# Kernel tuning notes

Measured on AMD Instinct MI355X. Metric: run time of the kernel, lower is better.

## Reference

```python
import jax, jax.numpy as jnp
import numpy as np
from jax import lax

# Problem sizes (see shape_source)
B, N, S, K = 16, 4096, 1024, 32   # clouds, points/cloud, fps samples/cloud, max neighbors
C_IN, H1, H2, C_OUT = 64, 64, 64, 128
R = 0.2                            # radius ball query radius


def setup_inputs() -> dict:
    key = jax.random.key(0)
    ks = jax.random.split(key, 6)
    x = jax.random.normal(ks[0], (B * N, C_IN), jnp.float32)
    pos = jax.random.uniform(ks[1], (B * N, 3), jnp.float32)  # unit cube
    batch = jnp.repeat(jnp.arange(B, dtype=jnp.int32), N)     # equal-size clouds
    def lin(k, fan_in, fan_out):
        return jax.random.normal(k, (fan_in, fan_out), jnp.float32) / np.float32(np.sqrt(fan_in))
    W1 = lin(ks[2], C_IN + 3, H1); b1 = jnp.zeros((H1,), jnp.float32)
    W2 = lin(ks[3], H1, H2);      b2 = jnp.zeros((H2,), jnp.float32)
    W3 = lin(ks[4], H2, C_OUT);   b3 = jnp.zeros((C_OUT,), jnp.float32)
    return dict(x=x, pos=pos, batch=batch, W1=W1, b1=b1, W2=W2, b2=b2, W3=W3, b3=b3)


def _fps_single(pos):
    """Farthest point sampling on one cloud. pos: [N,3] -> [S] int32 indices.
    Deterministic start at index 0 (random_start=False equivalent)."""
    def step(carry, _):
        mind, last = carry
        d = jnp.sum((pos - pos[last]) ** 2, axis=-1)   # [N]
        mind = jnp.minimum(mind, d)
        nxt = jnp.argmax(mind).astype(jnp.int32)
        return (mind, nxt), last
    init = (jnp.full((pos.shape[0],), jnp.inf, pos.dtype), jnp.int32(0))
    _, idx = lax.scan(step, init, None, length=S)
    return idx  # [S]


def _radius_single(pos, qpos):
    """Ball query: for each query return up to K in-radius neighbors (first K by
    point index, matching torch_cluster's 'first found' semantics).
    pos: [N,3], qpos: [S,3] -> (nbr [S,K] int32, mask [S,K] bool)."""
    d2 = jnp.sum((qpos[:, None, :] - pos[None, :, :]) ** 2, axis=-1)   # [S,N]
    valid = d2 <= R * R
    key = jnp.where(valid, jnp.arange(N, dtype=jnp.int32), jnp.int32(N))  # invalid -> sentinel N
    neg_key, nbr = lax.top_k(-key, K)        # K smallest keys == first K valid indices
    mask = (-neg_key) < N
    nbr = jnp.where(mask, nbr, 0).astype(jnp.int32)  # safe gather index
    return nbr, mask


def reference(x, pos, batch, W1, b1, W2, b2, W3, b3):
    xb = x.reshape(B, N, C_IN)
    posb = pos.reshape(B, N, 3)

    # 1) FPS sampling per cloud
    idx = jax.vmap(_fps_single)(posb)                                   # [B,S]
    qpos = jnp.take_along_axis(posb, idx[:, :, None], axis=1)           # [B,S,3]

    # 2) radius ball query (max 32 neighbors)
    nbr, mask = jax.vmap(_radius_single)(posb, qpos)                    # [B,S,K]

    # 3) PointNetConv: gather, relative pos, MLP, masked max-scatter
    flat = nbr.reshape(B, S * K)
    xj = jnp.take_along_axis(xb, flat[:, :, None], axis=1).reshape(B, S, K, C_IN)
    pj = jnp.take_along_axis(posb, flat[:, :, None], axis=1).reshape(B, S, K, 3)
    rel = pj - qpos[:, :, None, :]                                      # pos_j - pos_i
    h = jnp.concatenate([xj, rel], axis=-1)                             # [B,S,K,C_IN+3]
    h = jax.nn.relu(h @ W1 + b1)
    h = jax.nn.relu(h @ W2 + b2)
    h = h @ W3 + b3                                                     # [B,S,K,C_OUT]
    h = jnp.where(mask[..., None], h, -jnp.inf)
    agg = jnp.max(h, axis=2)                                            # max aggregation
    agg = jnp.where(jnp.any(mask, axis=2)[..., None], agg, 0.0)         # empty -> 0
    out = jax.nn.relu(agg)                                              # [B,S,C_OUT]

    new_batch = jnp.repeat(jnp.arange(B, dtype=batch.dtype), S)
    return out.reshape(B * S, C_OUT), qpos.reshape(B * S, 3), new_batch
```

## Files before the change

kernel.cpp:

```cpp
#include <hip/hip_runtime.h>
#include <cstdint>
#include <cstddef>

#define B_    16
#define N_    4096
#define S_    1024
#define K_    32
#define COUT_ 128
#define NQ_   (B_*S_)

#define NBLK_FPS  16
#define NBLK_XW   1024
#define NBLK_CONV 8192
#define GRID_     (NBLK_FPS + NBLK_XW + NBLK_CONV)

union __align__(16) SMem {
  struct {
    float px[N_], py[N_], pz[N_];
    int   hist[S_];
    unsigned long long wkey[2][4];
    float wx[2][4], wy[2][4], wz[2][4];
  } fps;
  struct {
    float xs[64*65];
    float ws[64*64];
  } xw;
  struct {
    float h1s[64*68];
    float h2s[64*68];
    float red[8*128];
    int   nbrs[64];
    float qps[8];
    int   cnts[2];
  } conv;
};

__device__ __forceinline__ uint64_t wave_max_u64_l63(uint64_t key) {
  uint32_t lo = (uint32_t)key, hi = (uint32_t)(key >> 32);
#define DPP_STEP(ctrl) { \
    uint32_t lo2 = (uint32_t)__builtin_amdgcn_update_dpp((int)lo, (int)lo, (ctrl), 0xf, 0xf, false); \
    uint32_t hi2 = (uint32_t)__builtin_amdgcn_update_dpp((int)hi, (int)hi, (ctrl), 0xf, 0xf, false); \
    const bool gt = (hi2 > hi) || (hi2 == hi && lo2 > lo); \
    hi = gt ? hi2 : hi; lo = gt ? lo2 : lo; \
  }
  DPP_STEP(0x111)
  DPP_STEP(0x112)
  DPP_STEP(0x114)
  DPP_STEP(0x118)
  DPP_STEP(0x142)
  DPP_STEP(0x143)
#undef DPP_STEP
  return ((uint64_t)hi << 32) | lo;
}

__device__ __forceinline__ void fps_role(
    SMem& sm, int b, const float* __restrict__ pos,
    float* __restrict__ qpos, float* __restrict__ batchf, int* progress)
{
  const int t = threadIdx.x;
  const int lane = t & 63, wid = t >> 6;
  const float* pb = pos + (size_t)b * N_ * 3;

  for (int i = t; i < N_; i += 256) {
    sm.fps.px[i] = pb[i*3+0]; sm.fps.py[i] = pb[i*3+1]; sm.fps.pz[i] = pb[i*3+2];
  }
  for (int s = t; s < S_; s += 256) batchf[(size_t)b*S_ + s] = (float)b;
  __syncthreads();

  float rx[16], ry[16], rz[16], mind[16];
  #pragma unroll
  for (int k = 0; k < 16; ++k) {
    const int p = k*256 + t;
    rx[k] = sm.fps.px[p]; ry[k] = sm.fps.py[p]; rz[k] = sm.fps.pz[p];
    mind[k] = INFINITY;
  }
  __builtin_amdgcn_s_setprio(2);

  int last = 0;
  float lx = sm.fps.px[0], ly = sm.fps.py[0], lz = sm.fps.pz[0];

  for (int s = 0; s < S_; ++s) {
    if (t == 0) sm.fps.hist[s] = last;
    if (s == S_-1) break;

    float bm = -1.0f; int kb = 0;
    #pragma unroll
    for (int k = 0; k < 16; ++k) {
      #pragma clang fp contract(off)
      const float dx = rx[k]-lx;
      const float dy = ry[k]-ly;
      const float dz = rz[k]-lz;
      const float d  = dx*dx + dy*dy + dz*dz;
      const float m  = fminf(mind[k], d);
      mind[k] = m;
      if (m > bm) { bm = m; kb = k; }
    }
    uint64_t key = ((uint64_t)__float_as_uint(bm) << 32)
                 | (uint32_t)((N_-1) - (kb*256 + t));
    key = wave_max_u64_l63(key);
    const int par = s & 1;
    if (lane == 63) {
      const int p = (N_-1) - (int)(uint32_t)key;
      sm.fps.wkey[par][wid] = key;
      sm.fps.wx[par][wid] = sm.fps.px[p];
      sm.fps.wy[par][wid] = sm.fps.py[p];
      sm.fps.wz[par][wid] = sm.fps.pz[p];
    }
    __syncthreads();
    {
      uint64_t k0 = sm.fps.wkey[par][0], k1 = sm.fps.wkey[par][1];
      uint64_t k2 = sm.fps.wkey[par][2], k3 = sm.fps.wkey[par][3];
      float x0=sm.fps.wx[par][0], x1=sm.fps.wx[par][1], x2=sm.fps.wx[par][2], x3=sm.fps.wx[par][3];
      float y0=sm.fps.wy[par][0], y1=sm.fps.wy[par][1], y2=sm.fps.wy[par][2], y3=sm.fps.wy[par][3];
      float z0=sm.fps.wz[par][0], z1=sm.fps.wz[par][1], z2=sm.fps.wz[par][2], z3=sm.fps.wz[par][3];
      if (k1 > k0) { k0=k1; x0=x1; y0=y1; z0=z1; }
      if (k3 > k2) { k2=k3; x2=x3; y2=y3; z2=z3; }
      if (k2 > k0) { k0=k2; x0=x2; y0=y2; z0=z2; }
      last = (N_-1) - (int)(uint32_t)k0;
      lx = x0; ly = y0; lz = z0;
    }
    if ((s & 31) == 31) {
      if (t < 32) {
        const int row = s - 31 + t;
        const int p = sm.fps.hist[row];
        const size_t o = ((size_t)b*S_ + row)*3;
        qpos[o+0] = sm.fps.px[p];
        qpos[o+1] = sm.fps.py[p];
        qpos[o+2] = sm.fps.pz[p];
      }
      if (t == 0)
        __hip_atomic_store(&progress[b], s+1, __ATOMIC_RELEASE, __HIP_MEMORY_SCOPE_AGENT);
    }
  }
  if (t < 32) {
    const int row = (S_-32) + t;
    const int p = sm.fps.hist[row];
    const size_t o = ((size_t)b*S_ + row)*3;
    qpos[o+0] = sm.fps.px[p];
    qpos[o+1] = sm.fps.py[p];
    qpos[o+2] = sm.fps.pz[p];
  }
  if (t == 0)
    __hip_atomic_store(&progress[b], S_, __ATOMIC_RELEASE, __HIP_MEMORY_SCOPE_AGENT);
}

__device__ __forceinline__ void xw_role(
    SMem& sm, int tile, const float* __restrict__ x,
    const float* __restrict__ W1, float* __restrict__ xw, int* xwdone)
{
  const int t = threadIdx.x;
  const size_t rowbase = (size_t)tile * 64;
  for (int k = t; k < 4096; k += 256) {
    sm.xw.xs[(k >> 6)*65 + (k & 63)] = x[rowbase*64 + k];
    sm.xw.ws[k] = W1[k];
  }
  __syncthreads();
  const int rg = t >> 4, cg = t & 15;
  const int r0 = rg*4, c0 = cg*4;
  float acc[4][4] = {};
  for (int i = 0; i < 64; ++i) {
    const float4 w = *(const float4*)&sm.xw.ws[i*64 + c0];
    #pragma unroll
    for (int j = 0; j < 4; ++j) {
      const float a = sm.xw.xs[(r0+j)*65 + i];
      acc[j][0] = fmaf(a, w.x, acc[j][0]);
      acc[j][1] = fmaf(a, w.y, acc[j][1]);
      acc[j][2] = fmaf(a, w.z, acc[j][2]);
      acc[j][3] = fmaf(a, w.w, acc[j][3]);
    }
  }
  #pragma unroll
  for (int j = 0; j < 4; ++j) {
    float4 v; v.x=acc[j][0]; v.y=acc[j][1]; v.z=acc[j][2]; v.w=acc[j][3];
    *(float4*)&xw[(rowbase + r0 + j)*64 + c0] = v;
  }
  __syncthreads();
  if (t == 0)
    __hip_atomic_fetch_add(&xwdone[tile >> 6], 1, __ATOMIC_RELEASE, __HIP_MEMORY_SCOPE_AGENT);
}

__device__ __forceinline__ void conv_role(
    SMem& sm, int j, const float* __restrict__ pos, const float* __restrict__ qpos,
    const float* __restrict__ xw,
    const float* __restrict__ W1, const float* __restrict__ b1,
    const float* __restrict__ W2, const float* __restrict__ b2,
    const float* __restrict__ W3, const float* __restrict__ b3,
    float* __restrict__ out, int* progress, int* xwdone)
{
  const int t = threadIdx.x;
  const int bb   = j & 15;
  const int pair = j >> 4;
  const int q0   = bb*S_ + pair*2;

  if (t == 0) {
    while (__hip_atomic_load(&xwdone[bb], __ATOMIC_ACQUIRE, __HIP_MEMORY_SCOPE_AGENT) < 64)
      __builtin_amdgcn_s_sleep(127);
    const int need = pair*2 + 2;
    while (__hip_atomic_load(&progress[bb], __ATOMIC_ACQUIRE, __HIP_MEMORY_SCOPE_AGENT) < need)
      __builtin_amdgcn_s_sleep(127);
  }
  __syncthreads();

  const int wid = t >> 6, lane = t & 63;
  if (wid < 2) {
    const int q = q0 + wid;
    const float* pb = pos + (size_t)bb * N_ * 3;
    const float qx = qpos[(size_t)q*3+0];
    const float qy = qpos[(size_t)q*3+1];
    const float qz = qpos[(size_t)q*3+2];
    int cnt = 0;
    for (int base = 0; base < N_; base += 64) {
      #pragma clang fp contract(off)
      const int i = base + lane;
      const float dx = qx - pb[i*3+0];
      const float dy = qy - pb[i*3+1];
      const float dz = qz - pb[i*3+2];
      const float d  = dx*dx + dy*dy + dz*dz;
      const bool valid = (d <= 0.04f);
      const unsigned long long bal = __ballot(valid);
      const int below = __popcll(bal & ((1ull << lane) - 1ull));
      const int p = cnt + below;
      if (valid && p < K_) sm.conv.nbrs[wid*K_ + p] = i;
      cnt += __popcll(bal);
      if (cnt >= K_) break;
    }
    const int c = (cnt < K_) ? cnt : K_;
    if (lane >= c && lane < K_) sm.conv.nbrs[wid*K_ + lane] = 0;
    if (lane == 0) sm.conv.cnts[wid] = c;
  }
  if (t < 6) sm.conv.qps[(t/3)*4 + (t%3)] = qpos[(size_t)q0*3 + t];
  __syncthreads();

  {
    const int c = t & 63;
    const int rsub = t >> 6;
    const float w1x = W1[64*64 + c];
    const float w1y = W1[65*64 + c];
    const float w1z = W1[66*64 + c];
    const float b1v = b1[c];
    #pragma unroll
    for (int it = 0; it < 16; ++it) {
      const int row = it*4 + rsub;
      const int lq  = row >> 5;
      const int jn  = sm.conv.nbrs[row];
      const size_t gp = (size_t)bb*N_ + jn;
      const float xv = xw[gp*64 + c];
      const float rx = pos[gp*3+0] - sm.conv.qps[lq*4+0];
      const float ry = pos[gp*3+1] - sm.conv.qps[lq*4+1];
      const float rz = pos[gp*3+2] - sm.conv.qps[lq*4+2];
      float h = fmaf(rx, w1x, xv);
      h = fmaf(ry, w1y, h);
      h = fmaf(rz, w1z, h);
      h += b1v;
      sm.conv.h1s[row*68 + c] = fmaxf(h, 0.0f);
    }
  }
  __syncthreads();

  {
    const int rg = t >> 4, cg = t & 15;
    const int r0 = rg*4, c0 = cg*4;
    float acc[4][4] = {};
    for (int i = 0; i < 64; i += 4) {
      float a[4][4];
      #pragma unroll
      for (int jj = 0; jj < 4; ++jj)
        *(float4*)&a[jj][0] = *(const float4*)&sm.conv.h1s[(r0+jj)*68 + i];
      #pragma unroll
      for (int di = 0; di < 4; ++di) {
        const float4 w = *(const float4*)&W2[(i+di)*64 + c0];
        #pragma unroll
        for (int jj = 0; jj < 4; ++jj) {
          const float av = a[jj][di];
          acc[jj][0] = fmaf(av, w.x, acc[jj][0]);
          acc[jj][1] = fmaf(av, w.y, acc[jj][1]);
          acc[jj][2] = fmaf(av, w.z, acc[jj][2]);
          acc[jj][3] = fmaf(av, w.w, acc[jj][3]);
        }
      }
    }
    const float4 bbv = *(const float4*)&b2[c0];
    #pragma unroll
    for (int jj = 0; jj < 4; ++jj) {
      float4 v;
      v.x = fmaxf(acc[jj][0] + bbv.x, 0.0f);
      v.y = fmaxf(acc[jj][1] + bbv.y, 0.0f);
      v.z = fmaxf(acc[jj][2] + bbv.z, 0.0f);
      v.w = fmaxf(acc[jj][3] + bbv.w, 0.0f);
      *(float4*)&sm.conv.h2s[(r0+jj)*68 + c0] = v;
    }
  }
  __syncthreads();

  {
    const int rg = t >> 5, cg = t & 31;
    const int r0 = rg*8, c0 = cg*4;
    const int lq = rg >> 2;
    const int cq = sm.conv.cnts[lq];
    float acc[8][4] = {};
    for (int i = 0; i < 64; i += 4) {
      float a[8][4];
      #pragma unroll
      for (int jj = 0; jj < 8; ++jj)
        *(float4*)&a[jj][0] = *(const float4*)&sm.conv.h2s[(r0+jj)*68 + i];
      #pragma unroll
      for (int di = 0; di < 4; ++di) {
        const float4 w = *(const float4*)&W3[(size_t)(i+di)*128 + c0];
        #pragma unroll
        for (int jj = 0; jj < 8; ++jj) {
          const float av = a[jj][di];
          acc[jj][0] = fmaf(av, w.x, acc[jj][0]);
          acc[jj][1] = fmaf(av, w.y, acc[jj][1]);
          acc[jj][2] = fmaf(av, w.z, acc[jj][2]);
          acc[jj][3] = fmaf(av, w.w, acc[jj][3]);
        }
      }
    }
    float pm0=-INFINITY, pm1=-INFINITY, pm2=-INFINITY, pm3=-INFINITY;
    #pragma unroll
    for (int jj = 0; jj < 8; ++jj) {
      const int n = (r0 + jj) & 31;
      if (n < cq) {
        pm0 = fmaxf(pm0, acc[jj][0]);
        pm1 = fmaxf(pm1, acc[jj][1]);
        pm2 = fmaxf(pm2, acc[jj][2]);
        pm3 = fmaxf(pm3, acc[jj][3]);
      }
    }
    float4 v; v.x=pm0; v.y=pm1; v.z=pm2; v.w=pm3;
    *(float4*)&sm.conv.red[rg*128 + c0] = v;
  }
  __syncthreads();
  {
    const int q = t >> 7, c = t & 127;
    const int cq = sm.conv.cnts[q];
    float v = -INFINITY;
    #pragma unroll
    for (int jj = 0; jj < 4; ++jj) v = fmaxf(v, sm.conv.red[(q*4+jj)*128 + c]);
    v = (cq > 0) ? (v + b3[c]) : 0.0f;
    v = fmaxf(v, 0.0f);
    out[(size_t)(q0 + q)*COUT_ + c] = v;
  }
}

__global__ __launch_bounds__(256) void mega_kernel(
    const float* __restrict__ x, const float* __restrict__ pos,
    const float* __restrict__ W1, const float* __restrict__ b1,
    const float* __restrict__ W2, const float* __restrict__ b2,
    const float* __restrict__ W3, const float* __restrict__ b3,
    float* __restrict__ out, float* __restrict__ qpos, float* __restrict__ batchf,
    float* __restrict__ xw, int* flags)
{
  __shared__ SMem sm;
  __shared__ int tk_s;
  int* ticket   = flags + 0;
  int* progress = flags + 16;
  int* xwdone   = flags + 48;
  if (threadIdx.x == 0) tk_s = atomicAdd(ticket, 1);
  __syncthreads();
  const int tk = tk_s;

  if (tk < NBLK_FPS) {
    fps_role(sm, tk, pos, qpos, batchf, progress);
  } else if (tk < NBLK_FPS + NBLK_XW) {
    xw_role(sm, tk - NBLK_FPS, x, W1, xw, xwdone);
  } else {
    conv_role(sm, tk - NBLK_FPS - NBLK_XW, pos, qpos, xw,
              W1, b1, W2, b2, W3, b3, out, progress, xwdone);
  }
}

extern "C" void kernel_launch(void* const* d_in, const int* in_sizes, int n_in,
                              void* d_out, int out_size, void* d_ws, size_t ws_size,
                              hipStream_t stream) {
  const float* x   = (const float*)d_in[0];
  const float* pos = (const float*)d_in[1];
  const float* W1  = (const float*)d_in[3];
  const float* b1  = (const float*)d_in[4];
  const float* W2  = (const float*)d_in[5];
  const float* b2  = (const float*)d_in[6];
  const float* W3  = (const float*)d_in[7];
  const float* b3  = (const float*)d_in[8];

  float* out    = (float*)d_out;
  float* qpos   = out + (size_t)NQ_*COUT_;
  float* batchf = qpos + (size_t)NQ_*3;

  char* ws = (char*)d_ws;
  float* xw  = (float*)ws;
  int* flags = (int*)(ws + (size_t)B_*N_*64*sizeof(float));

  hipMemsetAsync(flags, 0, 256, stream);
  hipLaunchKernelGGL(mega_kernel, dim3(GRID_), dim3(256), 0, stream,
                     x, pos, W1, b1, W2, b2, W3, b3, out, qpos, batchf, xw, flags);
}
```

Before: 1.020 ms.

## Convert mega-kernel to persistent workers with atomic work queues and dedicated FPS CUs

The launch drops from one block per task to 256 resident blocks. Sixteen of them run farthest point sampling; the rest pull XW tiles and then conv items from global atomic counters, waiting on the existing progress flags. The shared-memory union is padded to 88 KB, which limits each CU to one block, so the latency-bound FPS blocks no longer share a CU with conv work; the setprio hint is removed as a result. The cost is less latency hiding for the worker phases and the overhead of a serialized atomic counter for every work item.

```diff
diff --git a/kernel.cpp b/kernel.cpp
--- a/kernel.cpp
+++ b/kernel.cpp
@@ -9,10 +9,16 @@
 #define COUT_ 128
 #define NQ_   (B_*S_)
 
+#define NBLK_     256
 #define NBLK_FPS  16
-#define NBLK_XW   1024
-#define NBLK_CONV 8192
-#define GRID_     (NBLK_FPS + NBLK_XW + NBLK_CONV)
+#define NXW_TILES 1024
+#define NCONV_    8192
+
+#define F_TICKET 0
+#define F_PROG   16
+#define F_XWDONE 32
+#define F_XWCTR  64
+#define F_CVCTR  80
 
 union __align__(16) SMem {
   struct {
@@ -33,6 +39,7 @@
     float qps[8];
     int   cnts[2];
   } conv;
+  char pad[90112];
 };
 
 __device__ __forceinline__ uint64_t wave_max_u64_l63(uint64_t key) {
@@ -55,7 +62,7 @@
 
 __device__ __forceinline__ void fps_role(
     SMem& sm, int b, const float* __restrict__ pos,
-    float* __restrict__ qpos, float* __restrict__ batchf, int* progress)
+    float* __restrict__ qpos, float* __restrict__ batchf, volatile int* flags)
 {
   const int t = threadIdx.x;
   const int lane = t & 63, wid = t >> 6;
@@ -74,50 +81,49 @@
     rx[k] = sm.fps.px[p]; ry[k] = sm.fps.py[p]; rz[k] = sm.fps.pz[p];
     mind[k] = INFINITY;
   }
-  __builtin_amdgcn_s_setprio(2);
 
   int last = 0;
   float lx = sm.fps.px[0], ly = sm.fps.py[0], lz = sm.fps.pz[0];
 
   for (int s = 0; s < S_; ++s) {
     if (t == 0) sm.fps.hist[s] = last;
-    if (s == S_-1) break;
-
-    float bm = -1.0f; int kb = 0;
-    #pragma unroll
-    for (int k = 0; k < 16; ++k) {
-      #pragma clang fp contract(off)
-      const float dx = rx[k]-lx;
-      const float dy = ry[k]-ly;
-      const float dz = rz[k]-lz;
-      const float d  = dx*dx + dy*dy + dz*dz;
-      const float m  = fminf(mind[k], d);
-      mind[k] = m;
-      if (m > bm) { bm = m; kb = k; }
-    }
-    uint64_t key = ((uint64_t)__float_as_uint(bm) << 32)
-                 | (uint32_t)((N_-1) - (kb*256 + t));
-    key = wave_max_u64_l63(key);
-    const int par = s & 1;
-    if (lane == 63) {
-      const int p = (N_-1) - (int)(uint32_t)key;
-      sm.fps.wkey[par][wid] = key;
-      sm.fps.wx[par][wid] = sm.fps.px[p];
-      sm.fps.wy[par][wid] = sm.fps.py[p];
-      sm.fps.wz[par][wid] = sm.fps.pz[p];
-    }
-    __syncthreads();
-    {
-      uint64_t k0 = sm.fps.wkey[par][0], k1 = sm.fps.wkey[par][1];
-      uint64_t k2 = sm.fps.wkey[par][2], k3 = sm.fps.wkey[par][3];
-      float x0=sm.fps.wx[par][0], x1=sm.fps.wx[par][1], x2=sm.fps.wx[par][2], x3=sm.fps.wx[par][3];
-      float y0=sm.fps.wy[par][0], y1=sm.fps.wy[par][1], y2=sm.fps.wy[par][2], y3=sm.fps.wy[par][3];
-      float z0=sm.fps.wz[par][0], z1=sm.fps.wz[par][1], z2=sm.fps.wz[par][2], z3=sm.fps.wz[par][3];
-      if (k1 > k0) { k0=k1; x0=x1; y0=y1; z0=z1; }
-      if (k3 > k2) { k2=k3; x2=x3; y2=y3; z2=z3; }
-      if (k2 > k0) { k0=k2; x0=x2; y0=y2; z0=z2; }
-      last = (N_-1) - (int)(uint32_t)k0;
-      lx = x0; ly = y0; lz = z0;
+    if (s < S_-1) {
+      float bm = -1.0f; int kb = 0;
+      #pragma unroll
+      for (int k = 0; k < 16; ++k) {
+        #pragma clang fp contract(off)
+        const float dx = rx[k]-lx;
+        const float dy = ry[k]-ly;
+        const float dz = rz[k]-lz;
+        const float d  = dx*dx + dy*dy + dz*dz;
+        const float m  = fminf(mind[k], d);
+        mind[k] = m;
+        if (m > bm) { bm = m; kb = k; }
+      }
+      uint64_t key = ((uint64_t)__float_as_uint(bm) << 32)
+                   | (uint32_t)((N_-1) - (kb*256 + t));
+      key = wave_max_u64_l63(key);
+      const int par = s & 1;
+      if (lane == 63) {
+        const int p = (N_-1) - (int)(uint32_t)key;
+        sm.fps.wkey[par][wid] = key;
+        sm.fps.wx[par][wid] = sm.fps.px[p];
+        sm.fps.wy[par][wid] = sm.fps.py[p];
+        sm.fps.wz[par][wid] = sm.fps.pz[p];
+      }
+      __syncthreads();
+      {
+        uint64_t k0 = sm.fps.wkey[par][0], k1 = sm.fps.wkey[par][1];
+        uint64_t k2 = sm.fps.wkey[par][2], k3 = sm.fps.wkey[par][3];
+        float x0=sm.fps.wx[par][0], x1=sm.fps.wx[par][1], x2=sm.fps.wx[par][2], x3=sm.fps.wx[par][3];
+        float y0=sm.fps.wy[par][0], y1=sm.fps.wy[par][1], y2=sm.fps.wy[par][2], y3=sm.fps.wy[par][3];
+        float z0=sm.fps.wz[par][0], z1=sm.fps.wz[par][1], z2=sm.fps.wz[par][2], z3=sm.fps.wz[par][3];
+        if (k1 > k0) { k0=k1; x0=x1; y0=y1; z0=z1; }
+        if (k3 > k2) { k2=k3; x2=x3; y2=y3; z2=z3; }
+        if (k2 > k0) { k0=k2; x0=x2; y0=y2; z0=z2; }
+        last = (N_-1) - (int)(uint32_t)k0;
+        lx = x0; ly = y0; lz = z0;
+      }
     }
     if ((s & 31) == 31) {
       if (t < 32) {
@@ -129,24 +135,14 @@
         qpos[o+2] = sm.fps.pz[p];
       }
       if (t == 0)
-        __hip_atomic_store(&progress[b], s+1, __ATOMIC_RELEASE, __HIP_MEMORY_SCOPE_AGENT);
-    }
-  }
-  if (t < 32) {
-    const int row = (S_-32) + t;
-    const int p = sm.fps.hist[row];
-    const size_t o = ((size_t)b*S_ + row)*3;
-    qpos[o+0] = sm.fps.px[p];
-    qpos[o+1] = sm.fps.py[p];
-    qpos[o+2] = sm.fps.pz[p];
-  }
-  if (t == 0)
-    __hip_atomic_store(&progress[b], S_, __ATOMIC_RELEASE, __HIP_MEMORY_SCOPE_AGENT);
-}
-
-__device__ __forceinline__ void xw_role(
+        __hip_atomic_store((int*)&flags[F_PROG + b], s+1, __ATOMIC_RELEASE, __HIP_MEMORY_SCOPE_AGENT);
+    }
+  }
+}
+
+__device__ __forceinline__ void xw_tile_body(
     SMem& sm, int tile, const float* __restrict__ x,
-    const float* __restrict__ W1, float* __restrict__ xw, int* xwdone)
+    const float* __restrict__ W1, float* __restrict__ xw)
 {
   const int t = threadIdx.x;
   const size_t rowbase = (size_t)tile * 64;
@@ -174,34 +170,19 @@
     float4 v; v.x=acc[j][0]; v.y=acc[j][1]; v.z=acc[j][2]; v.w=acc[j][3];
     *(float4*)&xw[(rowbase + r0 + j)*64 + c0] = v;
   }
-  __syncthreads();
-  if (t == 0)
-    __hip_atomic_fetch_add(&xwdone[tile >> 6], 1, __ATOMIC_RELEASE, __HIP_MEMORY_SCOPE_AGENT);
-}
-
-__device__ __forceinline__ void conv_role(
-    SMem& sm, int j, const float* __restrict__ pos, const float* __restrict__ qpos,
+}
+
+__device__ __forceinline__ void conv_item_body(
+    SMem& sm, int bb, int q0, const float* __restrict__ pos, const float* __restrict__ qpos,
     const float* __restrict__ xw,
     const float* __restrict__ W1, const float* __restrict__ b1,
     const float* __restrict__ W2, const float* __restrict__ b2,
     const float* __restrict__ W3, const float* __restrict__ b3,
-    float* __restrict__ out, int* progress, int* xwdone)
+    float* __restrict__ out)
 {
   const int t = threadIdx.x;
-  const int bb   = j & 15;
-  const int pair = j >> 4;
-  const int q0   = bb*S_ + pair*2;
-
-  if (t == 0) {
-    while (__hip_atomic_load(&xwdone[bb], __ATOMIC_ACQUIRE, __HIP_MEMORY_SCOPE_AGENT) < 64)
-      __builtin_amdgcn_s_sleep(127);
-    const int need = pair*2 + 2;
-    while (__hip_atomic_load(&progress[bb], __ATOMIC_ACQUIRE, __HIP_MEMORY_SCOPE_AGENT) < need)
-      __builtin_amdgcn_s_sleep(127);
-  }
-  __syncthreads();
-
   const int wid = t >> 6, lane = t & 63;
+
   if (wid < 2) {
     const int q = q0 + wid;
     const float* pb = pos + (size_t)bb * N_ * 3;
@@ -245,12 +226,12 @@
       const int jn  = sm.conv.nbrs[row];
       const size_t gp = (size_t)bb*N_ + jn;
       const float xv = xw[gp*64 + c];
-      const float rx = pos[gp*3+0] - sm.conv.qps[lq*4+0];
-      const float ry = pos[gp*3+1] - sm.conv.qps[lq*4+1];
-      const float rz = pos[gp*3+2] - sm.conv.qps[lq*4+2];
-      float h = fmaf(rx, w1x, xv);
-      h = fmaf(ry, w1y, h);
-      h = fmaf(rz, w1z, h);
+      const float rxx = pos[gp*3+0] - sm.conv.qps[lq*4+0];
+      const float ryy = pos[gp*3+1] - sm.conv.qps[lq*4+1];
+      const float rzz = pos[gp*3+2] - sm.conv.qps[lq*4+2];
+      float h = fmaf(rxx, w1x, xv);
+      h = fmaf(ryy, w1y, h);
+      h = fmaf(rzz, w1z, h);
       h += b1v;
       sm.conv.h1s[row*68 + c] = fmaxf(h, 0.0f);
     }
@@ -343,6 +324,52 @@
   }
 }
 
+__device__ __forceinline__ void worker_role(
+    SMem& sm, int& slot_s,
+    const float* __restrict__ x, const float* __restrict__ pos,
+    const float* __restrict__ qpos, float* __restrict__ xw,
+    const float* __restrict__ W1, const float* __restrict__ b1,
+    const float* __restrict__ W2, const float* __restrict__ b2,
+    const float* __restrict__ W3, const float* __restrict__ b3,
+    float* __restrict__ out, int* flags)
+{
+  const int t = threadIdx.x;
+
+  for (;;) {
+    __syncthreads();
+    if (t == 0) slot_s = atomicAdd(&flags[F_XWCTR], 1);
+    __syncthreads();
+    const int tile = slot_s;
+    if (tile >= NXW_TILES) break;
+    xw_tile_body(sm, tile, x, W1, xw);
+    __syncthreads();
+    if (t == 0)
+      __hip_atomic_fetch_add(&flags[F_XWDONE + (tile >> 6)], 1, __ATOMIC_RELEASE, __HIP_MEMORY_SCOPE_AGENT);
+  }
+
+  for (;;) {
+    __syncthreads();
+    if (t == 0) {
+      const int it = atomicAdd(&flags[F_CVCTR], 1);
+      slot_s = it;
+      if (it < NCONV_) {
+        const int bb = it & 15, pair = it >> 4;
+        while (__hip_atomic_load(&flags[F_XWDONE + bb], __ATOMIC_ACQUIRE, __HIP_MEMORY_SCOPE_AGENT) < 64)
+          __builtin_amdgcn_s_sleep(32);
+        const int need = pair*2 + 2;
+        while (__hip_atomic_load(&flags[F_PROG + bb], __ATOMIC_ACQUIRE, __HIP_MEMORY_SCOPE_AGENT) < need)
+          __builtin_amdgcn_s_sleep(32);
+      }
+    }
+    __syncthreads();
+    const int item = slot_s;
+    if (item >= NCONV_) break;
+    const int bb = item & 15, pair = item >> 4;
+    conv_item_body(sm, bb, bb*S_ + pair*2, pos, qpos, xw,
+                   W1, b1, W2, b2, W3, b3, out);
+  }
+}
+
 __global__ __launch_bounds__(256) void mega_kernel(
     const float* __restrict__ x, const float* __restrict__ pos,
     const float* __restrict__ W1, const float* __restrict__ b1,
@@ -353,20 +380,15 @@
 {
   __shared__ SMem sm;
   __shared__ int tk_s;
-  int* ticket   = flags + 0;
-  int* progress = flags + 16;
-  int* xwdone   = flags + 48;
-  if (threadIdx.x == 0) tk_s = atomicAdd(ticket, 1);
+  __shared__ int slot_s;
+  if (threadIdx.x == 0) tk_s = atomicAdd(&flags[F_TICKET], 1);
   __syncthreads();
   const int tk = tk_s;
 
   if (tk < NBLK_FPS) {
-    fps_role(sm, tk, pos, qpos, batchf, progress);
-  } else if (tk < NBLK_FPS + NBLK_XW) {
-    xw_role(sm, tk - NBLK_FPS, x, W1, xw, xwdone);
+    fps_role(sm, tk, pos, qpos, batchf, flags);
   } else {
-    conv_role(sm, tk - NBLK_FPS - NBLK_XW, pos, qpos, xw,
-              W1, b1, W2, b2, W3, b3, out, progress, xwdone);
+    worker_role(sm, slot_s, x, pos, qpos, xw, W1, b1, W2, b2, W3, b3, out, flags);
   }
 }
 
@@ -390,7 +412,7 @@
   float* xw  = (float*)ws;
   int* flags = (int*)(ws + (size_t)B_*N_*64*sizeof(float));
 
-  hipMemsetAsync(flags, 0, 256, stream);
-  hipLaunchKernelGGL(mega_kernel, dim3(GRID_), dim3(256), 0, stream,
+  hipMemsetAsync(flags, 0, 512, stream);
+  hipLaunchKernelGGL(mega_kernel, dim3(NBLK_), dim3(256), 0, stream,
                      x, pos, W1, b1, W2, b2, W3, b3, out, qpos, batchf, xw, flags);
 }
```

Result: faster. 917.3 us (-10.1%).
